# Kernel tuning notes

Measured on AMD Instinct MI355X. Metric: run time of the kernel, lower is better.

## Reference

```python
import jax, jax.numpy as jnp
import numpy as np

N_NODES = 100000
N_EDGES = 1200000
IN_FEATS = 64
OUT_FEATS = 64


def setup_inputs() -> dict:
    key = jax.random.key(0)
    k1, k2, k3, k4 = jax.random.split(key, 4)
    feature = jax.random.normal(k1, (N_NODES, IN_FEATS), dtype=jnp.float32)
    edge_src = jax.random.randint(k2, (N_EDGES,), 0, N_NODES, dtype=jnp.int32)
    edge_dst = jax.random.randint(k3, (N_EDGES,), 0, N_NODES, dtype=jnp.int32)
    # xavier_normal_ init for linear weight (fan_in=fan_out=64)
    std = float(np.sqrt(2.0 / (IN_FEATS + OUT_FEATS)))
    W = jax.random.normal(k4, (OUT_FEATS, IN_FEATS), dtype=jnp.float32) * std
    b = jnp.zeros((OUT_FEATS,), dtype=jnp.float32)
    return {"feature": feature, "edge_src": edge_src, "edge_dst": edge_dst, "W": W, "b": b}


def reference(feature, edge_src, edge_dst, W, b):
    # copy_src: gather source-node features per edge, then mean-reduce by dst.
    msgs = feature[edge_src]                                   # [E, d_in]
    summed = jax.ops.segment_sum(msgs, edge_dst, num_segments=N_NODES)  # [N, d_in]
    deg = jax.ops.segment_sum(jnp.ones((edge_src.shape[0],), feature.dtype),
                              edge_dst, num_segments=N_NODES)  # [N]
    h = summed / jnp.maximum(deg, 1.0)[:, None]                # mean; 0 for isolated nodes
    # apply_nodes: linear + activation
    h = jnp.einsum("nd,od->no", h, W) + b
    return jax.nn.relu(h)
```

## Files before the change

### kernel.cpp

```cpp
#include <hip/hip_runtime.h>


typedef __attribute__((ext_vector_type(8))) short short8;
typedef __attribute__((ext_vector_type(4))) float floatx4;

constexpr int kNodes = 100000;
constexpr int kEdges = 1200000;

constexpr int kBuckets = 1024;
constexpr int kBucketNodes = 98;

constexpr int kBinBlocks = 128;
constexpr int kEdgesPerBlock = kEdges / kBinBlocks;
constexpr int kEPT = (kEdgesPerBlock + 1023) / 1024;

constexpr int kCap = 2048;
constexpr float kFxScale = 262144.0f;
constexpr int kAccStride = 68;

constexpr int kWsFeat   = 0;
constexpr int kWsOff    = 3200000;
constexpr int kWsBinned = kWsOff + kBinBlocks * (kBuckets + 1);

__device__ __forceinline__ unsigned bf16rne(float f) {
  unsigned u = __float_as_uint(f);
  return (u + 0x7fffu + ((u >> 16) & 1u)) >> 16;
}

__global__ __launch_bounds__(1024) void gcn_build(
    const float* __restrict__ feat,
    const int* __restrict__ src, const int* __restrict__ dst,
    int* __restrict__ ws) {
  uint2* fb16  = (uint2*)(ws + kWsFeat);
  int* offT   = ws + kWsOff;
  int* binned = ws + kWsBinned;

  __shared__ int lhist[kBuckets];
  __shared__ int sm[1024];
  __shared__ int lcur[kBuckets];

  const int tid = threadIdx.x;
  lhist[tid] = 0;
  __syncthreads();

  const int e0 = blockIdx.x * kEdgesPerBlock;
  int es[kEPT], ebk[kEPT], edl[kEPT];
  #pragma unroll
  for (int k = 0; k < kEPT; ++k) {
    const int j = tid + k * 1024;
    if (j < kEdgesPerBlock) {
      es[k] = src[e0 + j];
      const int d = dst[e0 + j];
      const int bk = d / kBucketNodes;
      ebk[k] = bk;
      edl[k] = d - bk * kBucketNodes;
      atomicAdd(&lhist[bk], 1);
    }
  }

  const int t = blockIdx.x * 1024 + tid;
  for (int i = t; i < kNodes * 16; i += kBinBlocks * 1024) {
    const float* fr = feat + (size_t)(i >> 4) * 64 + (i & 15);
    uint2 p;
    p.x = bf16rne(fr[0])  | (bf16rne(fr[16]) << 16);
    p.y = bf16rne(fr[32]) | (bf16rne(fr[48]) << 16);
    fb16[i] = p;
  }
  __syncthreads();

  const int own = lhist[tid];
  sm[tid] = own;
  __syncthreads();
  for (int off = 1; off < 1024; off <<= 1) {
    int v = (tid >= off) ? sm[tid - off] : 0;
    __syncthreads();
    sm[tid] += v;
    __syncthreads();
  }
  const int excl = sm[tid] - own;
  lcur[tid] = excl;
  offT[blockIdx.x * (kBuckets + 1) + tid] = excl;
  if (tid == 0) offT[blockIdx.x * (kBuckets + 1) + kBuckets] = kEdgesPerBlock;
  __syncthreads();

  int* myBin = binned + blockIdx.x * kEdgesPerBlock;
  #pragma unroll
  for (int k = 0; k < kEPT; ++k) {
    const int j = tid + k * 1024;
    if (j < kEdgesPerBlock) {
      const int pos = atomicAdd(&lcur[ebk[k]], 1);
      myBin[pos] = es[k] | (edl[k] << 17);
    }
  }
}

__global__ __launch_bounds__(1024) void gcn_aggregate(
    const int*   __restrict__ ws_in,
    const float* __restrict__ W,
    const float* __restrict__ b,
    float*       __restrict__ out) {
  const uint2* fb16  = (const uint2*)(ws_in + kWsFeat);
  const int* offT   = ws_in + kWsOff;
  const int* binned = ws_in + kWsBinned;

  __shared__ __align__(16) char uShared[112 * 72 * 2];
  __shared__ int    accum[kBucketNodes * kAccStride];
  __shared__ int    lofs[129];
  __shared__ int    lcur[128];
  __shared__ int    runL[kBinBlocks + 1];
  __shared__ int    runG[kBinBlocks];
  __shared__ int    ssm[kBinBlocks];
  __shared__ ushort Wb16[64 * 64];
  __shared__ float  bsh[64];
  int*    lsrc  = (int*)uShared;
  ushort* hsAll = (ushort*)uShared;

  const int tid = threadIdx.x;
  const int bkt = blockIdx.x;

  if (tid < 128) lcur[tid] = 0;
  for (int i = tid; i < 4096; i += 1024) Wb16[i] = (ushort)bf16rne(W[i]);
  if (tid < 64) bsh[tid] = b[tid];
  for (int i = tid; i < kBucketNodes * kAccStride; i += 1024) accum[i] = 0;

  int len = 0;
  if (tid < kBinBlocks) {
    const int o0 = offT[tid * (kBuckets + 1) + bkt];
    const int o1 = offT[tid * (kBuckets + 1) + bkt + 1];
    len = o1 - o0;
    runG[tid] = tid * kEdgesPerBlock + o0;
    ssm[tid] = len;
  }
  __syncthreads();
  for (int off = 1; off < kBinBlocks; off <<= 1) {
    int v = 0;
    if (tid < kBinBlocks && tid >= off) v = ssm[tid - off];
    __syncthreads();
    if (tid < kBinBlocks) ssm[tid] += v;
    __syncthreads();
  }
  if (tid < kBinBlocks) runL[tid] = ssm[tid] - len;
  if (tid == kBinBlocks - 1) runL[kBinBlocks] = ssm[kBinBlocks - 1];
  __syncthreads();

  int sz = runL[kBinBlocks];
  if (sz > kCap) sz = kCap;

  auto mapRead = [&](int j) -> unsigned {
    int lo = 0, hi = kBinBlocks;
    #pragma unroll
    for (int it = 0; it < 7; ++it) {
      const int mid = (lo + hi) >> 1;
      if (runL[mid] <= j) lo = mid; else hi = mid;
    }
    return (unsigned)binned[runG[lo] + (j - runL[lo])];
  };

  const int j0 = tid, j1 = tid + 1024;
  const bool va = j0 < sz, vb = j1 < sz;
  unsigned ea = 0, eb = 0;
  if (va) { ea = mapRead(j0); atomicAdd(&lcur[ea >> 17], 1); }
  if (vb) { eb = mapRead(j1); atomicAdd(&lcur[eb >> 17], 1); }
  __syncthreads();

  if (tid < 64) {
    const int a  = lcur[tid * 2];
    const int b2 = lcur[tid * 2 + 1];
    int s = a + b2;
    #pragma unroll
    for (int off = 1; off < 64; off <<= 1) {
      const int v = __shfl_up(s, off, 64);
      if (tid >= off) s += v;
    }
    const int ex1 = s - b2;
    const int ex0 = ex1 - a;
    lofs[tid * 2]     = ex0;
    lofs[tid * 2 + 1] = ex1;
    lcur[tid * 2]     = ex0;
    lcur[tid * 2 + 1] = ex1;
    if (tid == 63) lofs[128] = s;
  }
  __syncthreads();

  if (va) { const int p = atomicAdd(&lcur[ea >> 17], 1); lsrc[p] = (int)ea; }
  if (vb) { const int p = atomicAdd(&lcur[eb >> 17], 1); lsrc[p] = (int)eb; }
  __syncthreads();

  const int wave = tid >> 6;
  const int lane = tid & 63;
  const int g = lane >> 4;
  const int c = lane & 15;
  {
    const int slot = wave * 4 + g;
    const int jb = (sz * slot) >> 6;
    const int je = (sz * (slot + 1)) >> 6;
    for (int j = jb; j < je; ++j) {
      const unsigned e = (unsigned)lsrc[j];
      const int s  = (int)(e & 0x1FFFF);
      const int dL = (int)(e >> 17);
      const uint2 v = fb16[(size_t)s * 16 + c];
      int* row = accum + dL * kAccStride + c;
      atomicAdd(row + 0,  (int)(__uint_as_float(v.x << 16)          * kFxScale));
      atomicAdd(row + 16, (int)(__uint_as_float(v.x & 0xffff0000u) * kFxScale));
      atomicAdd(row + 32, (int)(__uint_as_float(v.y << 16)          * kFxScale));
      atomicAdd(row + 48, (int)(__uint_as_float(v.y & 0xffff0000u) * kFxScale));
    }
  }
  __syncthreads();

  {
    const int nd = tid >> 3;
    const int ch = tid & 7;
    if (nd < kBucketNodes) {
      const int dg = lofs[nd + 1] - lofs[nd];
      const float inv = 1.0f / (kFxScale * (float)(dg > 1 ? dg : 1));
      const int* arow = accum + nd * kAccStride + ch * 8;
      unsigned h[8];
      #pragma unroll
      for (int q = 0; q < 8; ++q) h[q] = bf16rne((float)arow[q] * inv);
      uint4 pk;
      pk.x = h[0] | (h[1] << 16);
      pk.y = h[2] | (h[3] << 16);
      pk.z = h[4] | (h[5] << 16);
      pk.w = h[6] | (h[7] << 16);
      *(uint4*)(hsAll + nd * 72 + ch * 8) = pk;
    } else {
      if (nd < 112) *(uint4*)(hsAll + nd * 72 + ch * 8) =
          make_uint4(0u, 0u, 0u, 0u);
    }
  }
  __syncthreads();

  if (tid < 448) {
    const int w8   = tid >> 6;
    const int ln   = tid & 63;
    const int quad = ln >> 4;
    const int col  = ln & 15;
    const int n0 = bkt * kBucketNodes;

    const short8 af0 = *reinterpret_cast<const short8*>(
        hsAll + (w8 * 16 + col) * 72 + 0 * 32 + quad * 8);
    const short8 af1 = *reinterpret_cast<const short8*>(
        hsAll + (w8 * 16 + col) * 72 + 1 * 32 + quad * 8);

    #pragma unroll
    for (int ob = 0; ob < 4; ++ob) {
      const short8 bf0 = *reinterpret_cast<const short8*>(
          Wb16 + (ob * 16 + col) * 64 + 0 * 32 + quad * 8);
      const short8 bf1 = *reinterpret_cast<const short8*>(
          Wb16 + (ob * 16 + col) * 64 + 1 * 32 + quad * 8);
      floatx4 acc = {0.f, 0.f, 0.f, 0.f};
      acc = __builtin_amdgcn_mfma_f32_16x16x32_bf16(af0, bf0, acc, 0, 0, 0);
      acc = __builtin_amdgcn_mfma_f32_16x16x32_bf16(af1, bf1, acc, 0, 0, 0);

      const int o = ob * 16 + col;
      const float bo = bsh[o];
      #pragma unroll
      for (int r = 0; r < 4; ++r) {
        const int local = w8 * 16 + quad * 4 + r;
        const int node = n0 + local;
        if (local < kBucketNodes && node < kNodes) {
          const float v = acc[r] + bo;
          out[(size_t)node * 64 + o] = v > 0.0f ? v : 0.0f;
        }
      }
    }
  }
}

extern "C" void kernel_launch(void* const* d_in, const int* in_sizes, int n_in,
                              void* d_out, int out_size, void* d_ws, size_t ws_size,
                              hipStream_t stream) {
  const float* feature  = (const float*)d_in[0];
  const int*   edge_src = (const int*)  d_in[1];
  const int*   edge_dst = (const int*)  d_in[2];
  const float* W        = (const float*)d_in[3];
  const float* b        = (const float*)d_in[4];

  float* out = (float*)d_out;
  int*   ws  = (int*)d_ws;

  gcn_build<<<kBinBlocks, 1024, 0, stream>>>(feature, edge_src, edge_dst, ws);
  gcn_aggregate<<<kBuckets, 1024, 0, stream>>>(ws, W, b, out);
}
```

Baseline: 137.8 us.

## Double bin blocks, use wave-shuffle scans, and run-accumulate edges before LDS atomics

```diff
diff --git a/kernel.cpp b/kernel.cpp
--- a/kernel.cpp
+++ b/kernel.cpp
@@ -10,8 +10,8 @@
 constexpr int kBuckets = 1024;
 constexpr int kBucketNodes = 98;
 
-constexpr int kBinBlocks = 128;
-constexpr int kEdgesPerBlock = kEdges / kBinBlocks;
+constexpr int kBinBlocks = 256;
+constexpr int kEdgesPerBlock = 4688;
 constexpr int kEPT = (kEdgesPerBlock + 1023) / 1024;
 
 constexpr int kCap = 2048;
@@ -31,24 +31,25 @@
     const float* __restrict__ feat,
     const int* __restrict__ src, const int* __restrict__ dst,
     int* __restrict__ ws) {
-  uint2* fb16  = (uint2*)(ws + kWsFeat);
+  uint2* fb16 = (uint2*)(ws + kWsFeat);
   int* offT   = ws + kWsOff;
   int* binned = ws + kWsBinned;
 
   __shared__ int lhist[kBuckets];
-  __shared__ int sm[1024];
   __shared__ int lcur[kBuckets];
+  __shared__ int wsum[16];
 
   const int tid = threadIdx.x;
   lhist[tid] = 0;
   __syncthreads();
 
   const int e0 = blockIdx.x * kEdgesPerBlock;
+  const int cnt = min(kEdgesPerBlock, kEdges - e0);
   int es[kEPT], ebk[kEPT], edl[kEPT];
   #pragma unroll
   for (int k = 0; k < kEPT; ++k) {
     const int j = tid + k * 1024;
-    if (j < kEdgesPerBlock) {
+    if (j < cnt) {
       es[k] = src[e0 + j];
       const int d = dst[e0 + j];
       const int bk = d / kBucketNodes;
@@ -69,37 +70,48 @@
   __syncthreads();
 
   const int own = lhist[tid];
-  sm[tid] = own;
-  __syncthreads();
-  for (int off = 1; off < 1024; off <<= 1) {
-    int v = (tid >= off) ? sm[tid - off] : 0;
-    __syncthreads();
-    sm[tid] += v;
-    __syncthreads();
-  }
-  const int excl = sm[tid] - own;
+  const int wv = tid >> 6, ln = tid & 63;
+  int sc = own;
+  #pragma unroll
+  for (int off = 1; off < 64; off <<= 1) {
+    const int v = __shfl_up(sc, off, 64);
+    if (ln >= off) sc += v;
+  }
+  if (ln == 63) wsum[wv] = sc;
+  __syncthreads();
+  if (tid < 64) {
+    int tw = (tid < 16) ? wsum[tid] : 0;
+    #pragma unroll
+    for (int off = 1; off < 16; off <<= 1) {
+      const int v = __shfl_up(tw, off, 64);
+      if (tid >= off) tw += v;
+    }
+    if (tid < 16) wsum[tid] = tw;
+  }
+  __syncthreads();
+  const int excl = sc - own + (wv ? wsum[wv - 1] : 0);
   lcur[tid] = excl;
   offT[blockIdx.x * (kBuckets + 1) + tid] = excl;
-  if (tid == 0) offT[blockIdx.x * (kBuckets + 1) + kBuckets] = kEdgesPerBlock;
+  if (tid == 0) offT[blockIdx.x * (kBuckets + 1) + kBuckets] = cnt;
   __syncthreads();
 
   int* myBin = binned + blockIdx.x * kEdgesPerBlock;
   #pragma unroll
   for (int k = 0; k < kEPT; ++k) {
     const int j = tid + k * 1024;
-    if (j < kEdgesPerBlock) {
+    if (j < cnt) {
       const int pos = atomicAdd(&lcur[ebk[k]], 1);
       myBin[pos] = es[k] | (edl[k] << 17);
     }
   }
 }
 
-__global__ __launch_bounds__(1024) void gcn_aggregate(
+__global__ __launch_bounds__(1024, 8) void gcn_aggregate(
     const int*   __restrict__ ws_in,
     const float* __restrict__ W,
     const float* __restrict__ b,
     float*       __restrict__ out) {
-  const uint2* fb16  = (const uint2*)(ws_in + kWsFeat);
+  const uint2* fb16 = (const uint2*)(ws_in + kWsFeat);
   const int* offT   = ws_in + kWsOff;
   const int* binned = ws_in + kWsBinned;
 
@@ -123,24 +135,31 @@
   if (tid < 64) bsh[tid] = b[tid];
   for (int i = tid; i < kBucketNodes * kAccStride; i += 1024) accum[i] = 0;
 
-  int len = 0;
   if (tid < kBinBlocks) {
     const int o0 = offT[tid * (kBuckets + 1) + bkt];
     const int o1 = offT[tid * (kBuckets + 1) + bkt + 1];
-    len = o1 - o0;
+    ssm[tid] = o1 - o0;
     runG[tid] = tid * kEdgesPerBlock + o0;
-    ssm[tid] = len;
-  }
-  __syncthreads();
-  for (int off = 1; off < kBinBlocks; off <<= 1) {
-    int v = 0;
-    if (tid < kBinBlocks && tid >= off) v = ssm[tid - off];
-    __syncthreads();
-    if (tid < kBinBlocks) ssm[tid] += v;
-    __syncthreads();
-  }
-  if (tid < kBinBlocks) runL[tid] = ssm[tid] - len;
-  if (tid == kBinBlocks - 1) runL[kBinBlocks] = ssm[kBinBlocks - 1];
+  }
+  __syncthreads();
+  if (tid < 64) {
+    const int base = tid * 4;
+    const int v0 = ssm[base], v1 = ssm[base + 1];
+    const int v2 = ssm[base + 2], v3 = ssm[base + 3];
+    const int p1 = v0 + v1, p2 = p1 + v2, tot = p2 + v3;
+    int sc = tot;
+    #pragma unroll
+    for (int off = 1; off < 64; off <<= 1) {
+      const int v = __shfl_up(sc, off, 64);
+      if (tid >= off) sc += v;
+    }
+    const int ex = sc - tot;
+    runL[base]     = ex;
+    runL[base + 1] = ex + v0;
+    runL[base + 2] = ex + p1;
+    runL[base + 3] = ex + p2;
+    if (tid == 63) runL[kBinBlocks] = sc;
+  }
   __syncthreads();
 
   int sz = runL[kBinBlocks];
@@ -149,7 +168,7 @@
   auto mapRead = [&](int j) -> unsigned {
     int lo = 0, hi = kBinBlocks;
     #pragma unroll
-    for (int it = 0; it < 7; ++it) {
+    for (int it = 0; it < 8; ++it) {
       const int mid = (lo + hi) >> 1;
       if (runL[mid] <= j) lo = mid; else hi = mid;
     }
@@ -194,16 +213,34 @@
     const int slot = wave * 4 + g;
     const int jb = (sz * slot) >> 6;
     const int je = (sz * (slot + 1)) >> 6;
+    int curDL = -1;
+    float a0 = 0.f, a1 = 0.f, a2 = 0.f, a3 = 0.f;
     for (int j = jb; j < je; ++j) {
       const unsigned e = (unsigned)lsrc[j];
-      const int s  = (int)(e & 0x1FFFF);
       const int dL = (int)(e >> 17);
-      const uint2 v = fb16[(size_t)s * 16 + c];
-      int* row = accum + dL * kAccStride + c;
-      atomicAdd(row + 0,  (int)(__uint_as_float(v.x << 16)          * kFxScale));
-      atomicAdd(row + 16, (int)(__uint_as_float(v.x & 0xffff0000u) * kFxScale));
-      atomicAdd(row + 32, (int)(__uint_as_float(v.y << 16)          * kFxScale));
-      atomicAdd(row + 48, (int)(__uint_as_float(v.y & 0xffff0000u) * kFxScale));
+      if (dL != curDL) {
+        if (curDL >= 0) {
+          int* row = accum + curDL * kAccStride + c;
+          atomicAdd(row + 0,  (int)(a0 * kFxScale));
+          atomicAdd(row + 16, (int)(a1 * kFxScale));
+          atomicAdd(row + 32, (int)(a2 * kFxScale));
+          atomicAdd(row + 48, (int)(a3 * kFxScale));
+        }
+        curDL = dL;
+        a0 = a1 = a2 = a3 = 0.f;
+      }
+      const uint2 v = fb16[(size_t)(e & 0x1FFFF) * 16 + c];
+      a0 += __uint_as_float(v.x << 16);
+      a1 += __uint_as_float(v.x & 0xffff0000u);
+      a2 += __uint_as_float(v.y << 16);
+      a3 += __uint_as_float(v.y & 0xffff0000u);
+    }
+    if (curDL >= 0) {
+      int* row = accum + curDL * kAccStride + c;
+      atomicAdd(row + 0,  (int)(a0 * kFxScale));
+      atomicAdd(row + 16, (int)(a1 * kFxScale));
+      atomicAdd(row + 32, (int)(a2 * kFxScale));
+      atomicAdd(row + 48, (int)(a3 * kFxScale));
     }
   }
   __syncthreads();
```

New measurement: 128.1 us. 1.08x faster.
